# Kernel optimization log

Measured on AMD Instinct MI355X. Metric: run time of the kernel, lower is better.

Reference implementation:

```python
import jax, jax.numpy as jnp
import numpy as np

B, S, D, H = 2, 2048, 1024, 16
DK = D // H

def setup_inputs() -> dict:
    key = jax.random.key(0)
    ks = jax.random.split(key, 11)
    scale = 0.02
    inp = {
        "Q": jax.random.normal(ks[0], (B, S, D), jnp.float32),
        "K": jax.random.normal(ks[1], (B, S, D), jnp.float32),
        "V": jax.random.normal(ks[2], (B, S, D), jnp.float32),
        "mask": jnp.ones((B, S), jnp.int32),
        "Wq": jax.random.normal(ks[3], (D, D), jnp.float32) * scale,
        "bq": jnp.zeros((D,), jnp.float32),
        "Wk": jax.random.normal(ks[4], (D, D), jnp.float32) * scale,
        "bk": jnp.zeros((D,), jnp.float32),
        "Wv": jax.random.normal(ks[5], (D, D), jnp.float32) * scale,
        "bv": jnp.zeros((D,), jnp.float32),
        "Wo": jax.random.normal(ks[6], (D, D), jnp.float32) * scale,
        "bo": jnp.zeros((D,), jnp.float32),
    }
    return inp

def _split_heads(x):
    # [B,S,D] -> [B,H,S,DK]
    return x.reshape(B, S, H, DK).transpose(0, 2, 1, 3)

def reference(Q, K, V, mask, Wq, bq, Wk, bk, Wv, bv, Wo, bo):
    q = _split_heads(Q @ Wq.T + bq)
    k = _split_heads(K @ Wk.T + bk)
    v = _split_heads(V @ Wv.T + bv)
    scores = jnp.einsum("bhqd,bhkd->bhqk", q, k) / jnp.sqrt(jnp.float32(DK))
    # 2D padding mask -> [B,1,1,S], mask==0 positions set to -inf
    m = mask[:, None, None, :]
    scores = jnp.where(m == 0, -jnp.inf, scores)
    attn_weights = jax.nn.softmax(scores, axis=-1)  # [B,H,S,S]
    attn_output = jnp.einsum("bhqk,bhkd->bhqd", attn_weights, v)
    attn_output = attn_output.transpose(0, 2, 1, 3).reshape(B, S, D)
    output = attn_output @ Wo.T + bo
    return (output, attn_weights)
```

## Files before the change

kernel.cpp:

```cpp
#include <hip/hip_runtime.h>
#include <stdint.h>

#define DEVINL __device__ __forceinline__

typedef float  f32x4  __attribute__((ext_vector_type(4)));
typedef float  f32x16 __attribute__((ext_vector_type(16)));
typedef short  s16x8  __attribute__((ext_vector_type(8)));
typedef unsigned short u16x8 __attribute__((ext_vector_type(8)));

static constexpr int Bb = 2, S = 2048, D = 1024, H = 16, DK = 64;
static constexpr size_t OUT0 = (size_t)Bb * S * D;

DEVINL unsigned short f2bf(float f) {
  union { float f; unsigned u; } v; v.f = f;
  unsigned r = v.u + 0x7FFFu + ((v.u >> 16) & 1u);
  return (unsigned short)(r >> 16);
}

DEVINL unsigned cvt_pk_bf16(float lo, float hi) {
  unsigned r;
  asm("v_cvt_pk_bf16_f32 %0, %1, %2" : "=v"(r) : "v"(lo), "v"(hi));
  return r;
}

DEVINL void perm32swap(unsigned& a, unsigned& b) {
#if __has_builtin(__builtin_amdgcn_permlane32_swap)
  auto r = __builtin_amdgcn_permlane32_swap(a, b, false, false);
  a = r[0]; b = r[1];
#else
  asm volatile("v_permlane32_swap_b32 %0, %1" : "+v"(a), "+v"(b));
#endif
}

DEVINL void gload_lds16(const void* g, void* l) {
  __builtin_amdgcn_global_load_lds(
      (const __attribute__((address_space(1))) unsigned int*)g,
      (__attribute__((address_space(3))) unsigned int*)l, 16, 0, 0);
}

DEVINL void cvt_body(const float* __restrict__ src, unsigned short* __restrict__ dst, int i) {
  const f32x4* s4 = (const f32x4*)src;
  f32x4 a = s4[i * 2], b = s4[i * 2 + 1];
  u16x8 o;
  o[0] = f2bf(a[0]); o[1] = f2bf(a[1]); o[2] = f2bf(a[2]); o[3] = f2bf(a[3]);
  o[4] = f2bf(b[0]); o[5] = f2bf(b[1]); o[6] = f2bf(b[2]); o[7] = f2bf(b[3]);
  ((u16x8*)dst)[i] = o;
}

__global__ __launch_bounds__(256) void k_cvt3(const float* __restrict__ a, const float* __restrict__ b,
                                              const float* __restrict__ c,
                                              unsigned short* __restrict__ oa, unsigned short* __restrict__ ob,
                                              unsigned short* __restrict__ oc) {
  int z = blockIdx.y;
  const float* src = z == 0 ? a : z == 1 ? b : c;
  unsigned short* dst = z == 0 ? oa : z == 1 ? ob : oc;
  cvt_body(src, dst, blockIdx.x * 256 + threadIdx.x);
}

__global__ __launch_bounds__(256) void k_cvt4(const float* __restrict__ a, const float* __restrict__ b,
                                              const float* __restrict__ c, const float* __restrict__ d,
                                              unsigned short* __restrict__ oa, unsigned short* __restrict__ ob,
                                              unsigned short* __restrict__ oc, unsigned short* __restrict__ od) {
  int z = blockIdx.y;
  const float* src = z == 0 ? a : z == 1 ? b : z == 2 ? c : d;
  unsigned short* dst = z == 0 ? oa : z == 1 ? ob : z == 2 ? oc : od;
  cvt_body(src, dst, blockIdx.x * 256 + threadIdx.x);
}

template <int MODE>
DEVINL void gemm_tile(const unsigned short* __restrict__ A,
                      const unsigned short* __restrict__ Bw,
                      const float* __restrict__ bias, void* __restrict__ Cout,
                      int tileM, int tileN, float scl,
                      unsigned short* As, unsigned short* Bs) {
  const int tid = threadIdx.x;
  const int lane = tid & 63, wave = tid >> 6;
  const int wr = wave >> 1, wc = wave & 1;
  const int l15 = lane & 15, l16 = lane >> 4;
  f32x4 acc[4][4] = {};
  for (int k0 = 0; k0 < 1024; k0 += 32) {
#pragma unroll
    for (int p = 0; p < 2; ++p) {
      int c = tid + p * 256;
      int row = c >> 2, col = (c & 3) * 8;
      gload_lds16(A + (((size_t)(tileM + row)) << 10) + k0 + col, &As[c * 8]);
      gload_lds16(Bw + (((size_t)(tileN + row)) << 10) + k0 + col, &Bs[c * 8]);
    }
    __syncthreads();
    s16x8 af[4], bf[4];
#pragma unroll
    for (int i = 0; i < 4; ++i)
      af[i] = *(const s16x8*)&As[(wr * 64 + i * 16 + l15) * 32 + l16 * 8];
#pragma unroll
    for (int i = 0; i < 4; ++i)
      bf[i] = *(const s16x8*)&Bs[(wc * 64 + i * 16 + l15) * 32 + l16 * 8];
#pragma unroll
    for (int i = 0; i < 4; ++i)
#pragma unroll
      for (int j = 0; j < 4; ++j)
        acc[i][j] = __builtin_amdgcn_mfma_f32_16x16x32_bf16(af[i], bf[j], acc[i][j], 0, 0, 0);
    __syncthreads();
  }
#pragma unroll
  for (int i = 0; i < 4; ++i) {
#pragma unroll
    for (int j = 0; j < 4; ++j) {
      int n = tileN + wc * 64 + j * 16 + l15;
      float bv = bias[n];
#pragma unroll
      for (int r = 0; r < 4; ++r) {
        int m = tileM + wr * 64 + i * 16 + l16 * 4 + r;
        float v = (acc[i][j][r] + bv) * scl;
        if (MODE == 0) {
          int b_ = m >> 11, s_ = m & 2047, h_ = n >> 6, d_ = n & 63;
          ((unsigned short*)Cout)[(((size_t)(b_ * H + h_) * S) + s_) * DK + d_] = f2bf(v);
        } else {
          ((float*)Cout)[(size_t)m * 1024 + n] = v;
        }
      }
    }
  }
}

__global__ __launch_bounds__(256) void k_gemm_qkv(
    const unsigned short* __restrict__ Xq, const unsigned short* __restrict__ Xk,
    const unsigned short* __restrict__ Xv,
    const unsigned short* __restrict__ Wq, const unsigned short* __restrict__ Wk,
    const unsigned short* __restrict__ Wv,
    const float* __restrict__ bq, const float* __restrict__ bk, const float* __restrict__ bv,
    unsigned short* __restrict__ oq, unsigned short* __restrict__ ok, unsigned short* __restrict__ ov) {
  __shared__ alignas(16) unsigned short As[128 * 32];
  __shared__ alignas(16) unsigned short Bs[128 * 32];
  int flat = (blockIdx.z * 32 + blockIdx.y) * 8 + blockIdx.x;
  int swz = (flat & 7) * 96 + (flat >> 3);
  int z = swz >> 8;
  int rem = swz & 255;
  int ty = rem >> 3, tx = rem & 7;
  const unsigned short* A = z == 0 ? Xq : z == 1 ? Xk : Xv;
  const unsigned short* W = z == 0 ? Wq : z == 1 ? Wk : Wv;
  const float* bias = z == 0 ? bq : z == 1 ? bk : bv;
  unsigned short* o = z == 0 ? oq : z == 1 ? ok : ov;
  float scl = z == 0 ? 0.125f : 1.0f;
  gemm_tile<0>(A, W, bias, o, ty * 128, tx * 128, scl, As, Bs);
}

__global__ __launch_bounds__(256) void k_gemm_out(const unsigned short* __restrict__ A,
                                                  const unsigned short* __restrict__ W,
                                                  const float* __restrict__ bias,
                                                  float* __restrict__ Cout) {
  __shared__ alignas(16) unsigned short As[128 * 32];
  __shared__ alignas(16) unsigned short Bs[128 * 32];
  int flat = blockIdx.y * 8 + blockIdx.x;
  int swz = (flat & 7) * 32 + (flat >> 3);
  int ty = swz >> 3, tx = swz & 7;
  gemm_tile<1>(A, W, bias, Cout, ty * 128, tx * 128, 1.0f, As, Bs);
}

__global__ __launch_bounds__(256) void k_transpose_v(const unsigned short* __restrict__ vstd,
                                                     unsigned short* __restrict__ vt2) {
  __shared__ alignas(16) unsigned short T[64][72];
  int bh = blockIdx.y, st = blockIdx.x;
  int t = threadIdx.x;
  int rr = t >> 3, cc = (t & 7) * 8;
#pragma unroll
  for (int i = 0; i < 2; ++i) {
    int r = rr + i * 32;
    u16x8 v = *(const u16x8*)&vstd[((size_t)bh * S + st * 64 + r) * 64 + cc];
    *(u16x8*)&T[r][cc] = v;
  }
  __syncthreads();
#pragma unroll
  for (int i = 0; i < 2; ++i) {
    int d = rr + i * 32;
    u16x8 o;
#pragma unroll
    for (int j = 0; j < 8; ++j) o[j] = T[cc + j][d];
    *(u16x8*)&vt2[(size_t)bh * S * 64 + st * 4096 + d * 64 + cc] = o;
  }
}

__global__ __launch_bounds__(256) void k_attn_fused(const unsigned short* __restrict__ qw,
                                                    const unsigned short* __restrict__ kw,
                                                    const unsigned short* __restrict__ vt2,
                                                    const int* __restrict__ mask,
                                                    unsigned short* __restrict__ aout,
                                                    float* __restrict__ attw) {
  __shared__ alignas(16) char lds[33536];
  unsigned short* Ks = (unsigned short*)lds;
  unsigned short* Vs = (unsigned short*)(lds + 16384);
  float* lsumW = (float*)(lds + 32768);
  float* lsumT = (float*)(lds + 33280);
  float* nl2lW = (float*)(lds + 33408);
  const float LOG2E = 1.44269504f;

  int flat = blockIdx.y * 64 + blockIdx.x;
  int swzb = (flat & 7) * 256 + (flat >> 3);
  const int bh = swzb >> 6, b = bh >> 4, h = bh & 15;
  const int q0 = (swzb & 63) * 32;
  const int tid = threadIdx.x;
  const int lane = tid & 63, w = tid >> 6;
  const int l31 = lane & 31, hi = lane >> 5;

  const unsigned short* kw_bh = kw + (size_t)bh * S * 64;
  const unsigned short* vt_bh = vt2 + (size_t)bh * S * 64;
  const int* mrow = mask + b * S;

  s16x8 qf[4];
  const unsigned short* qbase = qw + ((size_t)bh * S + q0 + l31) * 64 + hi * 8;
#pragma unroll
  for (int kc = 0; kc < 4; ++kc) qf[kc] = *(const s16x8*)(qbase + kc * 16);

  f32x16 oT0 = {}, oT1 = {};
  float lsum = 0.f;
  const int swv = (l31 & 15) << 4;

  for (int t = 0; t < 16; ++t) {
#pragma unroll
    for (int p = 0; p < 4; ++p) {
      int c = tid + p * 256, row = c >> 3, cc = (c & 7) ^ (row & 7);
      gload_lds16(kw_bh + ((size_t)(t * 128 + row)) * 64 + cc * 8, Ks + c * 8);
    }
#pragma unroll
    for (int p = 0; p < 4; ++p) {
      int c = tid + p * 256, row = c >> 4, c16 = (c & 15) ^ (row & 15);
      gload_lds16(vt_bh + (size_t)(t * 2 + (c16 >> 3)) * 4096 + row * 64 + (c16 & 7) * 8,
                  Vs + c * 8);
    }
    __syncthreads();

    const int krow = w * 32 + l31;
    f32x16 sT = {};
#pragma unroll
    for (int kc = 0; kc < 4; ++kc) {
      s16x8 ka = *(const s16x8*)((const char*)Ks + krow * 128 +
                                 ((kc * 32 + hi * 16) ^ ((krow & 7) << 4)));
      sT = __builtin_amdgcn_mfma_f32_32x32x16_bf16(ka, qf[kc], sT, 0, 0, 0);
    }

    int base = t * 128 + w * 32 + 4 * hi;
    int m[16];
    *(int4*)&m[0]  = *(const int4*)&mrow[base];
    *(int4*)&m[4]  = *(const int4*)&mrow[base + 8];
    *(int4*)&m[8]  = *(const int4*)&mrow[base + 16];
    *(int4*)&m[12] = *(const int4*)&mrow[base + 24];

    float e[16];
#pragma unroll
    for (int r = 0; r < 16; ++r) {
      e[r] = m[r] ? exp2f(sT[r] * LOG2E) : 0.f;
      lsum += e[r];
    }

    unsigned x0 = cvt_pk_bf16(e[0], e[1]),   x1 = cvt_pk_bf16(e[2], e[3]);
    unsigned x2 = cvt_pk_bf16(e[4], e[5]),   x3 = cvt_pk_bf16(e[6], e[7]);
    unsigned x4 = cvt_pk_bf16(e[8], e[9]),   x5 = cvt_pk_bf16(e[10], e[11]);
    unsigned x6 = cvt_pk_bf16(e[12], e[13]), x7 = cvt_pk_bf16(e[14], e[15]);
    perm32swap(x0, x2); perm32swap(x1, x3);
    perm32swap(x4, x6); perm32swap(x5, x7);
    union { unsigned u[4]; s16x8 v; } p0u, p1u;
    p0u.u[0] = x0; p0u.u[1] = x1; p0u.u[2] = x2; p0u.u[3] = x3;
    p1u.u[0] = x4; p1u.u[1] = x5; p1u.u[2] = x6; p1u.u[3] = x7;

    const int ko0 = w * 64 + hi * 16, ko1 = w * 64 + 32 + hi * 16;
    const char* Vr0 = (const char*)Vs + l31 * 256;
    const char* Vr1 = (const char*)Vs + (32 + l31) * 256;
    s16x8 va;
    va = *(const s16x8*)(Vr0 + (ko0 ^ swv));
    oT0 = __builtin_amdgcn_mfma_f32_32x32x16_bf16(va, p0u.v, oT0, 0, 0, 0);
    va = *(const s16x8*)(Vr0 + (ko1 ^ swv));
    oT0 = __builtin_amdgcn_mfma_f32_32x32x16_bf16(va, p1u.v, oT0, 0, 0, 0);
    va = *(const s16x8*)(Vr1 + (ko0 ^ swv));
    oT1 = __builtin_amdgcn_mfma_f32_32x32x16_bf16(va, p0u.v, oT1, 0, 0, 0);
    va = *(const s16x8*)(Vr1 + (ko1 ^ swv));
    oT1 = __builtin_amdgcn_mfma_f32_32x32x16_bf16(va, p1u.v, oT1, 0, 0, 0);

    __syncthreads();
  }

  lsum += __shfl_xor(lsum, 32);
  if (hi == 0) lsumW[w * 32 + l31] = lsum;

  {
    char* orow = (char*)lds + w * 8192 + l31 * 256;
#pragma unroll
    for (int rg = 0; rg < 4; ++rg) {
      f32x4 c0, c1;
#pragma unroll
      for (int j = 0; j < 4; ++j) { c0[j] = oT0[rg * 4 + j]; c1[j] = oT1[rg * 4 + j]; }
      *(f32x4*)(orow + ((rg * 32 + hi * 16) ^ swv)) = c0;
      *(f32x4*)(orow + ((128 + rg * 32 + hi * 16) ^ swv)) = c1;
    }
  }
  __syncthreads();

  if (tid < 32) {
    float tot = lsumW[tid] + lsumW[32 + tid] + lsumW[64 + tid] + lsumW[96 + tid];
    lsumT[tid] = tot;
    nl2lW[tid] = __log2f(tot);
  }
  __syncthreads();

  {
    int q = tid >> 3, dg = tid & 7;
    float inv = 1.f / lsumT[q];
    int sq = (q & 15) << 4;
    float s[8] = {};
#pragma unroll
    for (int w4 = 0; w4 < 4; ++w4) {
      const char* prow = (const char*)lds + w4 * 8192 + q * 256;
      f32x4 a = *(const f32x4*)(prow + ((dg * 32) ^ sq));
      f32x4 bb = *(const f32x4*)(prow + ((dg * 32 + 16) ^ sq));
#pragma unroll
      for (int j = 0; j < 4; ++j) { s[j] += a[j]; s[4 + j] += bb[j]; }
    }
    u16x8 ob;
#pragma unroll
    for (int j = 0; j < 8; ++j) ob[j] = f2bf(s[j] * inv);
    *(u16x8*)&aout[((size_t)b * S + q0 + q) * D + h * 64 + dg * 8] = ob;
  }

  float nl2l[16];
#pragma unroll
  for (int r = 0; r < 16; ++r) nl2l[r] = nl2lW[(r & 3) + 8 * (r >> 2) + 4 * hi];

  for (int it = 0; it < 16; ++it) {
    int key0 = it * 128 + w * 32;
    const unsigned short* kbase = kw_bh + (size_t)(key0 + l31) * 64 + hi * 8;
    s16x8 kb[4];
#pragma unroll
    for (int kc = 0; kc < 4; ++kc) kb[kc] = *(const s16x8*)(kbase + kc * 16);
    f32x16 dacc = {};
#pragma unroll
    for (int kc = 0; kc < 4; ++kc)
      dacc = __builtin_amdgcn_mfma_f32_32x32x16_bf16(qf[kc], kb[kc], dacc, 0, 0, 0);

    int key = key0 + l31;
    int mk = mrow[key];
    float* obase = attw + ((size_t)bh * S + q0) * S + key;
#pragma unroll
    for (int r = 0; r < 16; ++r) {
      int row = (r & 3) + 8 * (r >> 2) + 4 * hi;
      float wv = mk ? exp2f(dacc[r] * LOG2E - nl2l[r]) : 0.f;
      __builtin_nontemporal_store(wv, obase + (size_t)row * S);
    }
  }
}

extern "C" void kernel_launch(void* const* d_in, const int* in_sizes, int n_in,
                              void* d_out, int out_size, void* d_ws, size_t ws_size,
                              hipStream_t stream) {
  (void)in_sizes; (void)n_in; (void)out_size; (void)ws_size;
  const float* Q  = (const float*)d_in[0];
  const float* K  = (const float*)d_in[1];
  const float* V  = (const float*)d_in[2];
  const int* mask = (const int*)d_in[3];
  const float* Wq = (const float*)d_in[4];
  const float* bq = (const float*)d_in[5];
  const float* Wk = (const float*)d_in[6];
  const float* bk = (const float*)d_in[7];
  const float* Wv = (const float*)d_in[8];
  const float* bv = (const float*)d_in[9];
  const float* Wo = (const float*)d_in[10];
  const float* bo = (const float*)d_in[11];

  char* ws = (char*)d_ws;
  unsigned short* Xbf  = (unsigned short*)(ws + 0);
  unsigned short* Wbf  = (unsigned short*)(ws + 25165824);
  unsigned short* qws  = (unsigned short*)(ws + 33554432);
  unsigned short* kws  = (unsigned short*)(ws + 41943040);
  unsigned short* vstd = (unsigned short*)(ws + 50331648);
  unsigned short* vt2  = (unsigned short*)(ws + 0);
  unsigned short* aoutb= (unsigned short*)(ws + 8388608);
  float* out0 = (float*)d_out;
  float* attw = (float*)d_out + OUT0;

  k_cvt3<<<dim3(2048, 3), dim3(256), 0, stream>>>(Q, K, V, Xbf, Xbf + 4194304, Xbf + 8388608);
  k_cvt4<<<dim3(512, 4), dim3(256), 0, stream>>>(Wq, Wk, Wv, Wo,
                                                 Wbf, Wbf + 1048576, Wbf + 2097152, Wbf + 3145728);

  k_gemm_qkv<<<dim3(8, 32, 3), dim3(256), 0, stream>>>(
      Xbf, Xbf + 4194304, Xbf + 8388608,
      Wbf, Wbf + 1048576, Wbf + 2097152,
      bq, bk, bv, qws, kws, vstd);

  k_transpose_v<<<dim3(32, 32), dim3(256), 0, stream>>>(vstd, vt2);

  k_attn_fused<<<dim3(64, 32), dim3(256), 0, stream>>>(qws, kws, vt2, mask, aoutb, attw);

  k_gemm_out<<<dim3(8, 32), dim3(256), 0, stream>>>(aoutb, Wbf + 3145728, bo, out0);
}
```

Baseline: 247.5 us.

## Merge conversion kernels, swizzle GEMM LDS with K=64 tiles, fuse V transpose

Combines the two fp32-to-bf16 conversion launches into one grid. Doubles the GEMM K-tile to 64 and XOR-swizzles the LDS layout to avoid bank conflicts, which halves the number of barrier pairs. The V projection now writes directly in the transposed blocked layout that attention consumes, so the separate transpose kernel and its round trip through memory are removed. In exchange, LDS use per block doubles, which may reduce occupancy.

```diff
diff --git a/kernel.cpp b/kernel.cpp
--- a/kernel.cpp
+++ b/kernel.cpp
@@ -6,10 +6,11 @@
 typedef float  f32x4  __attribute__((ext_vector_type(4)));
 typedef float  f32x16 __attribute__((ext_vector_type(16)));
 typedef short  s16x8  __attribute__((ext_vector_type(8)));
+typedef unsigned short u16x4 __attribute__((ext_vector_type(4)));
 typedef unsigned short u16x8 __attribute__((ext_vector_type(8)));
 
-static constexpr int Bb = 2, S = 2048, D = 1024, H = 16, DK = 64;
-static constexpr size_t OUT0 = (size_t)Bb * S * D;
+static constexpr int S = 2048, D = 1024, H = 16;
+static constexpr size_t OUT0 = (size_t)2 * S * D;
 
 DEVINL unsigned short f2bf(float f) {
   union { float f; unsigned u; } v; v.f = f;
@@ -47,24 +48,28 @@
   ((u16x8*)dst)[i] = o;
 }
 
-__global__ __launch_bounds__(256) void k_cvt3(const float* __restrict__ a, const float* __restrict__ b,
-                                              const float* __restrict__ c,
-                                              unsigned short* __restrict__ oa, unsigned short* __restrict__ ob,
-                                              unsigned short* __restrict__ oc) {
-  int z = blockIdx.y;
-  const float* src = z == 0 ? a : z == 1 ? b : c;
-  unsigned short* dst = z == 0 ? oa : z == 1 ? ob : oc;
-  cvt_body(src, dst, blockIdx.x * 256 + threadIdx.x);
-}
-
-__global__ __launch_bounds__(256) void k_cvt4(const float* __restrict__ a, const float* __restrict__ b,
-                                              const float* __restrict__ c, const float* __restrict__ d,
-                                              unsigned short* __restrict__ oa, unsigned short* __restrict__ ob,
-                                              unsigned short* __restrict__ oc, unsigned short* __restrict__ od) {
-  int z = blockIdx.y;
-  const float* src = z == 0 ? a : z == 1 ? b : z == 2 ? c : d;
-  unsigned short* dst = z == 0 ? oa : z == 1 ? ob : z == 2 ? oc : od;
-  cvt_body(src, dst, blockIdx.x * 256 + threadIdx.x);
+__global__ __launch_bounds__(256) void k_cvt_all(
+    const float* __restrict__ Q, const float* __restrict__ K, const float* __restrict__ V,
+    const float* __restrict__ Wq, const float* __restrict__ Wk,
+    const float* __restrict__ Wv, const float* __restrict__ Wo,
+    unsigned short* __restrict__ Xq, unsigned short* __restrict__ Xk,
+    unsigned short* __restrict__ Xv,
+    unsigned short* __restrict__ WQ, unsigned short* __restrict__ WK,
+    unsigned short* __restrict__ WV, unsigned short* __restrict__ WO) {
+  int i = blockIdx.x;
+  const float* src; unsigned short* dst; int item;
+  if (i < 6144) {
+    int z = i >> 11;
+    item = (i & 2047) * 256 + threadIdx.x;
+    src = z == 0 ? Q : z == 1 ? K : V;
+    dst = z == 0 ? Xq : z == 1 ? Xk : Xv;
+  } else {
+    int j = i - 6144, z = j >> 9;
+    item = (j & 511) * 256 + threadIdx.x;
+    src = z == 0 ? Wq : z == 1 ? Wk : z == 2 ? Wv : Wo;
+    dst = z == 0 ? WQ : z == 1 ? WK : z == 2 ? WV : WO;
+  }
+  cvt_body(src, dst, item);
 }
 
 template <int MODE>
@@ -78,27 +83,36 @@
   const int wr = wave >> 1, wc = wave & 1;
   const int l15 = lane & 15, l16 = lane >> 4;
   f32x4 acc[4][4] = {};
-  for (int k0 = 0; k0 < 1024; k0 += 32) {
-#pragma unroll
-    for (int p = 0; p < 2; ++p) {
+  for (int k0 = 0; k0 < 1024; k0 += 64) {
+#pragma unroll
+    for (int p = 0; p < 4; ++p) {
       int c = tid + p * 256;
-      int row = c >> 2, col = (c & 3) * 8;
-      gload_lds16(A + (((size_t)(tileM + row)) << 10) + k0 + col, &As[c * 8]);
-      gload_lds16(Bw + (((size_t)(tileN + row)) << 10) + k0 + col, &Bs[c * 8]);
+      int row = c >> 3, cc = (c & 7) ^ (row & 7);
+      gload_lds16(A + (((size_t)(tileM + row)) << 10) + k0 + cc * 8, &As[c * 8]);
+      gload_lds16(Bw + (((size_t)(tileN + row)) << 10) + k0 + cc * 8, &Bs[c * 8]);
     }
     __syncthreads();
-    s16x8 af[4], bf[4];
-#pragma unroll
-    for (int i = 0; i < 4; ++i)
-      af[i] = *(const s16x8*)&As[(wr * 64 + i * 16 + l15) * 32 + l16 * 8];
-#pragma unroll
-    for (int i = 0; i < 4; ++i)
-      bf[i] = *(const s16x8*)&Bs[(wc * 64 + i * 16 + l15) * 32 + l16 * 8];
-#pragma unroll
-    for (int i = 0; i < 4; ++i)
-#pragma unroll
-      for (int j = 0; j < 4; ++j)
-        acc[i][j] = __builtin_amdgcn_mfma_f32_16x16x32_bf16(af[i], bf[j], acc[i][j], 0, 0, 0);
+#pragma unroll
+    for (int kk = 0; kk < 2; ++kk) {
+      s16x8 af[4], bf[4];
+#pragma unroll
+      for (int i = 0; i < 4; ++i) {
+        int r = wr * 64 + i * 16 + l15;
+        af[i] = *(const s16x8*)((const char*)As + r * 128 +
+                                ((kk * 64 + l16 * 16) ^ ((r & 7) << 4)));
+      }
+#pragma unroll
+      for (int j = 0; j < 4; ++j) {
+        int r = wc * 64 + j * 16 + l15;
+        bf[j] = *(const s16x8*)((const char*)Bs + r * 128 +
+                                ((kk * 64 + l16 * 16) ^ ((r & 7) << 4)));
+      }
+#pragma unroll
+      for (int i = 0; i < 4; ++i)
+#pragma unroll
+        for (int j = 0; j < 4; ++j)
+          acc[i][j] = __builtin_amdgcn_mfma_f32_16x16x32_bf16(af[i], bf[j], acc[i][j], 0, 0, 0);
+    }
     __syncthreads();
   }
 #pragma unroll
@@ -107,15 +121,26 @@
     for (int j = 0; j < 4; ++j) {
       int n = tileN + wc * 64 + j * 16 + l15;
       float bv = bias[n];
-#pragma unroll
-      for (int r = 0; r < 4; ++r) {
-        int m = tileM + wr * 64 + i * 16 + l16 * 4 + r;
-        float v = (acc[i][j][r] + bv) * scl;
-        if (MODE == 0) {
-          int b_ = m >> 11, s_ = m & 2047, h_ = n >> 6, d_ = n & 63;
-          ((unsigned short*)Cout)[(((size_t)(b_ * H + h_) * S) + s_) * DK + d_] = f2bf(v);
-        } else {
-          ((float*)Cout)[(size_t)m * 1024 + n] = v;
+      if (MODE == 2) {
+        int m0 = tileM + wr * 64 + i * 16 + l16 * 4;
+        int b_ = m0 >> 11, s_ = m0 & 2047;
+        int h_ = n >> 6, d_ = n & 63;
+        u16x4 o;
+#pragma unroll
+        for (int r = 0; r < 4; ++r) o[r] = f2bf(acc[i][j][r] + bv);
+        *(u16x4*)&((unsigned short*)Cout)[(size_t)(b_ * H + h_) * S * 64 +
+                                          (s_ >> 6) * 4096 + d_ * 64 + (s_ & 63)] = o;
+      } else {
+#pragma unroll
+        for (int r = 0; r < 4; ++r) {
+          int m = tileM + wr * 64 + i * 16 + l16 * 4 + r;
+          float v = (acc[i][j][r] + bv) * scl;
+          if (MODE == 0) {
+            int b_ = m >> 11, s_ = m & 2047, h_ = n >> 6, d_ = n & 63;
+            ((unsigned short*)Cout)[(((size_t)(b_ * H + h_) * S) + s_) * 64 + d_] = f2bf(v);
+          } else {
+            ((float*)Cout)[(size_t)m * 1024 + n] = v;
+          }
         }
       }
     }
@@ -128,55 +153,36 @@
     const unsigned short* __restrict__ Wq, const unsigned short* __restrict__ Wk,
     const unsigned short* __restrict__ Wv,
     const float* __restrict__ bq, const float* __restrict__ bk, const float* __restrict__ bv,
-    unsigned short* __restrict__ oq, unsigned short* __restrict__ ok, unsigned short* __restrict__ ov) {
-  __shared__ alignas(16) unsigned short As[128 * 32];
-  __shared__ alignas(16) unsigned short Bs[128 * 32];
+    unsigned short* __restrict__ oq, unsigned short* __restrict__ ok,
+    unsigned short* __restrict__ vt2) {
+  __shared__ alignas(16) unsigned short As[128 * 64];
+  __shared__ alignas(16) unsigned short Bs[128 * 64];
   int flat = (blockIdx.z * 32 + blockIdx.y) * 8 + blockIdx.x;
   int swz = (flat & 7) * 96 + (flat >> 3);
   int z = swz >> 8;
   int rem = swz & 255;
   int ty = rem >> 3, tx = rem & 7;
-  const unsigned short* A = z == 0 ? Xq : z == 1 ? Xk : Xv;
-  const unsigned short* W = z == 0 ? Wq : z == 1 ? Wk : Wv;
-  const float* bias = z == 0 ? bq : z == 1 ? bk : bv;
-  unsigned short* o = z == 0 ? oq : z == 1 ? ok : ov;
-  float scl = z == 0 ? 0.125f : 1.0f;
-  gemm_tile<0>(A, W, bias, o, ty * 128, tx * 128, scl, As, Bs);
+  if (z == 2) {
+    gemm_tile<2>(Xv, Wv, bv, vt2, ty * 128, tx * 128, 1.0f, As, Bs);
+  } else {
+    const unsigned short* A = z == 0 ? Xq : Xk;
+    const unsigned short* W = z == 0 ? Wq : Wk;
+    const float* bias = z == 0 ? bq : bk;
+    unsigned short* o = z == 0 ? oq : ok;
+    gemm_tile<0>(A, W, bias, o, ty * 128, tx * 128, z == 0 ? 0.125f : 1.0f, As, Bs);
+  }
 }
 
 __global__ __launch_bounds__(256) void k_gemm_out(const unsigned short* __restrict__ A,
                                                   const unsigned short* __restrict__ W,
                                                   const float* __restrict__ bias,
                                                   float* __restrict__ Cout) {
-  __shared__ alignas(16) unsigned short As[128 * 32];
-  __shared__ alignas(16) unsigned short Bs[128 * 32];
+  __shared__ alignas(16) unsigned short As[128 * 64];
+  __shared__ alignas(16) unsigned short Bs[128 * 64];
   int flat = blockIdx.y * 8 + blockIdx.x;
   int swz = (flat & 7) * 32 + (flat >> 3);
   int ty = swz >> 3, tx = swz & 7;
   gemm_tile<1>(A, W, bias, Cout, ty * 128, tx * 128, 1.0f, As, Bs);
-}
-
-__global__ __launch_bounds__(256) void k_transpose_v(const unsigned short* __restrict__ vstd,
-                                                     unsigned short* __restrict__ vt2) {
-  __shared__ alignas(16) unsigned short T[64][72];
-  int bh = blockIdx.y, st = blockIdx.x;
-  int t = threadIdx.x;
-  int rr = t >> 3, cc = (t & 7) * 8;
-#pragma unroll
-  for (int i = 0; i < 2; ++i) {
-    int r = rr + i * 32;
-    u16x8 v = *(const u16x8*)&vstd[((size_t)bh * S + st * 64 + r) * 64 + cc];
-    *(u16x8*)&T[r][cc] = v;
-  }
-  __syncthreads();
-#pragma unroll
-  for (int i = 0; i < 2; ++i) {
-    int d = rr + i * 32;
-    u16x8 o;
-#pragma unroll
-    for (int j = 0; j < 8; ++j) o[j] = T[cc + j][d];
-    *(u16x8*)&vt2[(size_t)bh * S * 64 + st * 4096 + d * 64 + cc] = o;
-  }
 }
 
 __global__ __launch_bounds__(256) void k_attn_fused(const unsigned short* __restrict__ qw,
@@ -368,22 +374,20 @@
   unsigned short* Wbf  = (unsigned short*)(ws + 25165824);
   unsigned short* qws  = (unsigned short*)(ws + 33554432);
   unsigned short* kws  = (unsigned short*)(ws + 41943040);
-  unsigned short* vstd = (unsigned short*)(ws + 50331648);
-  unsigned short* vt2  = (unsigned short*)(ws + 0);
+  unsigned short* vt2  = (unsigned short*)(ws + 50331648);
   unsigned short* aoutb= (unsigned short*)(ws + 8388608);
   float* out0 = (float*)d_out;
   float* attw = (float*)d_out + OUT0;
 
-  k_cvt3<<<dim3(2048, 3), dim3(256), 0, stream>>>(Q, K, V, Xbf, Xbf + 4194304, Xbf + 8388608);
-  k_cvt4<<<dim3(512, 4), dim3(256), 0, stream>>>(Wq, Wk, Wv, Wo,
-                                                 Wbf, Wbf + 1048576, Wbf + 2097152, Wbf + 3145728);
+  k_cvt_all<<<dim3(8192), dim3(256), 0, stream>>>(
+      Q, K, V, Wq, Wk, Wv, Wo,
+      Xbf, Xbf + 4194304, Xbf + 8388608,
+      Wbf, Wbf + 1048576, Wbf + 2097152, Wbf + 3145728);
 
   k_gemm_qkv<<<dim3(8, 32, 3), dim3(256), 0, stream>>>(
       Xbf, Xbf + 4194304, Xbf + 8388608,
       Wbf, Wbf + 1048576, Wbf + 2097152,
-      bq, bk, bv, qws, kws, vstd);
-
-  k_transpose_v<<<dim3(32, 32), dim3(256), 0, stream>>>(vstd, vt2);
+      bq, bk, bv, qws, kws, vt2);
 
   k_attn_fused<<<dim3(64, 32), dim3(256), 0, stream>>>(qws, kws, vt2, mask, aoutb, attw);
 
```

New measurement: 250.5 us. Within noise of the previous version (+1.2%).
